# Performance work log

Measured on AMD Instinct MI355X. Metric: run time of the kernel, lower is better.

The kernel has to match this reference:

```python
import jax, jax.numpy as jnp
import numpy as np

SQRT_D = 32  # ceil(sqrt(d_out)) with d_out = 1024
D_OUT = 1024


def setup_inputs() -> dict:
    key = jax.random.key(0)
    k1, k2, k3 = jax.random.split(key, 3)
    x = jax.random.normal(k1, (8, 4096, 1024), dtype=jnp.float32)
    scale = 1.0 / np.sqrt(SQRT_D)
    L = jax.random.normal(k2, (SQRT_D, SQRT_D, SQRT_D), dtype=jnp.float32) * scale
    R = jax.random.normal(k3, (SQRT_D, SQRT_D, SQRT_D), dtype=jnp.float32) * scale
    return {"x": x, "L": L, "R": R}


def reference(x, L, R):
    # MonarchOutProjection with proj_type == 'Monarch' (d_in*n_heads == d_out,
    # hd == sqrt_d**2 so no padding). Monarch: permute -> blockdiag(L) ->
    # permute -> blockdiag(R) -> permute, then slice to d_out.
    b, n, hd = x.shape
    s = SQRT_D
    # rearrange '... (m n) -> ... (n m)': view (m, n) then transpose.
    h = x.reshape(b, n, s, s)          # (..., m, n_inner)
    h = jnp.swapaxes(h, -1, -2)        # (..., block, inner)
    # blockdiag_matmul with L: einsum 'bnm,...bm->...bn'
    h = jnp.einsum('bnm,...bm->...bn', L, h)
    # rearrange '... (m n) -> ... (n m)' on the flattened result == transpose
    h = jnp.swapaxes(h, -1, -2)
    # blockdiag_matmul with R
    h = jnp.einsum('bnm,...bm->...bn', R, h)
    # final rearrange '... (m n) -> ... (n m)'
    h = jnp.swapaxes(h, -1, -2)
    out = h.reshape(b, n, hd)
    return out[..., :D_OUT]
```

## Files before the change

### kernel.cpp

```cpp
#include <hip/hip_runtime.h>
#include <hip/hip_bf16.h>


typedef __attribute__((ext_vector_type(8))) short short8;
typedef __attribute__((ext_vector_type(4))) float floatx4;

__device__ __forceinline__ unsigned int f2bf(float f) {
    unsigned int u = __float_as_uint(f);
    return (u + 0x7fffu + ((u >> 16) & 1u)) >> 16;
}
__device__ __forceinline__ unsigned int pack2bf(float a, float b) {
    __hip_bfloat162 h = __float22bfloat162_rn(float2{a, b});
    return *(unsigned int*)&h;
}
__device__ __forceinline__ float bf2f(unsigned int u16) {
    return __uint_as_float(u16 << 16);
}

__global__ void prep_weights(const float* __restrict__ L, const float* __restrict__ R,
                             unsigned short* __restrict__ Lb, unsigned short* __restrict__ Rb) {
    const int t = blockIdx.x * 256 + threadIdx.x;
    const float* src        = (t < 4096) ? L : R;
    unsigned short* dst     = (t < 4096) ? Lb : Rb;
    const int i    = t & 4095;
    const int lane = i & 63;
    const int pq   = i >> 6;
    const int p    = pq >> 1;
    const int qt   = pq & 1;
    const int q    = qt * 16 + (lane & 15);
    const int m0   = (lane >> 4) * 8;
    const float* s = src + (p * 32 + q) * 32 + m0;
    uint4 o;
    o.x = pack2bf(s[0], s[1]);
    o.y = pack2bf(s[2], s[3]);
    o.z = pack2bf(s[4], s[5]);
    o.w = pack2bf(s[6], s[7]);
    *(uint4*)(dst + (size_t)i * 8) = o;
}

__global__ __launch_bounds__(256, 4)
void monarch_kernel(const float* __restrict__ x,
                    const unsigned short* __restrict__ Lb,
                    const unsigned short* __restrict__ Rb,
                    float* __restrict__ out) {
    __shared__ __align__(16) unsigned short buf[16][1024];

    const int tid  = threadIdx.x;
    const int w    = tid >> 6;
    const int lane = tid & 63;
    const int tl   = lane & 15;
    const int quad = lane >> 4;
    const long tok0 = (long)blockIdx.x * 16;

    {
        const int c = tid * 4;
        #pragma unroll
        for (int t = 0; t < 16; ++t) {
            const float4 v = *(const float4*)(x + (tok0 + t) * 1024 + c);
            *(unsigned int*)&buf[t][(c    ) ^ (2 * t)] = pack2bf(v.x, v.y);
            *(unsigned int*)&buf[t][(c + 2) ^ (2 * t)] = pack2bf(v.z, v.w);
        }
    }
    __syncthreads();

    {
        const int xsw = 2 * tl;
        #pragma unroll
        for (int pp = 0; pp < 8; ++pp) {
            const int p  = w * 8 + pp;
            const int pX = p ^ xsw;
            short8 b1;
            #pragma unroll
            for (int j = 0; j < 8; ++j)
                b1[j] = (short)buf[tl][quad * 256 + j * 32 + pX];
            #pragma unroll
            for (int qt = 0; qt < 2; ++qt) {
                const short8 a1 = *(const short8*)(Lb + (size_t)((p * 2 + qt) * 64 + lane) * 8);
                floatx4 acc = {0.f, 0.f, 0.f, 0.f};
                acc = __builtin_amdgcn_mfma_f32_16x16x32_bf16(a1, b1, acc, 0, 0, 0);
                #pragma unroll
                for (int r = 0; r < 4; ++r) {
                    const int qo = qt * 16 + quad * 4 + r;
                    buf[tl][qo * 32 + pX] = (unsigned short)f2bf(acc[r]);
                }
            }
        }
    }
    __syncthreads();

    floatx4 acc2[8][2];
    {
        const int xsw = 2 * tl;
        #pragma unroll
        for (int qq = 0; qq < 8; ++qq) {
            const int q = w * 8 + qq;
            short8 b2;
            #pragma unroll
            for (int j = 0; j < 8; ++j)
                b2[j] = (short)buf[tl][q * 32 + ((quad * 8 + j) ^ xsw)];
            #pragma unroll
            for (int rt = 0; rt < 2; ++rt) {
                const short8 a2 = *(const short8*)(Rb + (size_t)((q * 2 + rt) * 64 + lane) * 8);
                floatx4 z = {0.f, 0.f, 0.f, 0.f};
                acc2[qq][rt] = __builtin_amdgcn_mfma_f32_16x16x32_bf16(a2, b2, z, 0, 0, 0);
            }
        }
    }
    __syncthreads();

    {
        const int xsw = 2 * tl;
        #pragma unroll
        for (int qq = 0; qq < 8; ++qq) {
            const int q  = w * 8 + qq;
            const int qX = q ^ xsw;
            #pragma unroll
            for (int rt = 0; rt < 2; ++rt) {
                #pragma unroll
                for (int r4 = 0; r4 < 4; ++r4) {
                    const int ro = rt * 16 + quad * 4 + r4;
                    buf[tl][ro * 32 + qX] = (unsigned short)f2bf(acc2[qq][rt][r4]);
                }
            }
        }
    }
    __syncthreads();

    {
        const int c = tid * 4;
        #pragma unroll
        for (int t = 0; t < 16; ++t) {
            const unsigned int u0 = *(const unsigned int*)&buf[t][(c    ) ^ (2 * t)];
            const unsigned int u1 = *(const unsigned int*)&buf[t][(c + 2) ^ (2 * t)];
            float4 o;
            o.x = bf2f(u0 & 0xffffu); o.y = bf2f(u0 >> 16);
            o.z = bf2f(u1 & 0xffffu); o.w = bf2f(u1 >> 16);
            *(float4*)(out + (tok0 + t) * 1024 + c) = o;
        }
    }
}

extern "C" void kernel_launch(void* const* d_in, const int* in_sizes, int n_in,
                              void* d_out, int out_size, void* d_ws, size_t ws_size,
                              hipStream_t stream) {
    const float* x = (const float*)d_in[0];
    const float* L = (const float*)d_in[1];
    const float* R = (const float*)d_in[2];
    float* out = (float*)d_out;

    unsigned short* Lb = (unsigned short*)d_ws;
    unsigned short* Rb = Lb + 32768;

    prep_weights<<<32, 256, 0, stream>>>(L, R, Lb, Rb);

    const int n_tokens = 8 * 4096;
    const int grid = n_tokens / 16;
    monarch_kernel<<<grid, 256, 0, stream>>>(x, Lb, Rb, out);
}
```

Measured before the change: 242.1 us.

## Process two token tiles per block and prefetch the next tile's input during compute

Each block now handles 32 tokens in two iterations. The block loads the first tile's x into registers up front and issues the second tile's global loads during the first tile's second-stage matmul, which overlaps memory latency with compute. Stage-two results are packed to bf16 in registers, and the bf16 pack routine is swapped to a manual rounding version. The cost is more register pressure from 16 float4 values held across the loop, plus a halved grid, which may reduce occupancy and latency hiding under the 4-block launch bound.

```diff
diff --git a/kernel.cpp b/kernel.cpp
--- a/kernel.cpp
+++ b/kernel.cpp
@@ -10,8 +10,7 @@
     return (u + 0x7fffu + ((u >> 16) & 1u)) >> 16;
 }
 __device__ __forceinline__ unsigned int pack2bf(float a, float b) {
-    __hip_bfloat162 h = __float22bfloat162_rn(float2{a, b});
-    return *(unsigned int*)&h;
+    return f2bf(a) | (f2bf(b) << 16);
 }
 __device__ __forceinline__ float bf2f(unsigned int u16) {
     return __uint_as_float(u16 << 16);
@@ -50,84 +49,102 @@
     const int lane = tid & 63;
     const int tl   = lane & 15;
     const int quad = lane >> 4;
-    const long tok0 = (long)blockIdx.x * 16;
+    const int c    = tid * 4;
+    const long tokB = (long)blockIdx.x * 32;
 
-    {
-        const int c = tid * 4;
+    float4 v[16];
+    #pragma unroll
+    for (int t = 0; t < 16; ++t)
+        v[t] = *(const float4*)(x + (tokB + t) * 1024 + c);
+
+    #pragma unroll 1
+    for (int it = 0; it < 2; ++it) {
+        const long tok0 = tokB + it * 16;
+
         #pragma unroll
         for (int t = 0; t < 16; ++t) {
-            const float4 v = *(const float4*)(x + (tok0 + t) * 1024 + c);
-            *(unsigned int*)&buf[t][(c    ) ^ (2 * t)] = pack2bf(v.x, v.y);
-            *(unsigned int*)&buf[t][(c + 2) ^ (2 * t)] = pack2bf(v.z, v.w);
+            *(unsigned int*)&buf[t][(c    ) ^ (2 * t)] = pack2bf(v[t].x, v[t].y);
+            *(unsigned int*)&buf[t][(c + 2) ^ (2 * t)] = pack2bf(v[t].z, v[t].w);
         }
-    }
-    __syncthreads();
+        __syncthreads();
 
-    {
-        const int xsw = 2 * tl;
-        #pragma unroll
-        for (int pp = 0; pp < 8; ++pp) {
-            const int p  = w * 8 + pp;
-            const int pX = p ^ xsw;
-            short8 b1;
+        {
+            const int xsw = 2 * tl;
             #pragma unroll
-            for (int j = 0; j < 8; ++j)
-                b1[j] = (short)buf[tl][quad * 256 + j * 32 + pX];
-            #pragma unroll
-            for (int qt = 0; qt < 2; ++qt) {
-                const short8 a1 = *(const short8*)(Lb + (size_t)((p * 2 + qt) * 64 + lane) * 8);
-                floatx4 acc = {0.f, 0.f, 0.f, 0.f};
-                acc = __builtin_amdgcn_mfma_f32_16x16x32_bf16(a1, b1, acc, 0, 0, 0);
+            for (int pp = 0; pp < 8; ++pp) {
+                const int p  = w * 8 + pp;
+                const int pX = p ^ xsw;
+                short8 b1;
                 #pragma unroll
-                for (int r = 0; r < 4; ++r) {
-                    const int qo = qt * 16 + quad * 4 + r;
-                    buf[tl][qo * 32 + pX] = (unsigned short)f2bf(acc[r]);
+                for (int j = 0; j < 8; ++j)
+                    b1[j] = (short)buf[tl][quad * 256 + j * 32 + pX];
+                #pragma unroll
+                for (int qt = 0; qt < 2; ++qt) {
+                    const short8 a1 = *(const short8*)(Lb + (size_t)((p * 2 + qt) * 64 + lane) * 8);
+                    floatx4 acc = {0.f, 0.f, 0.f, 0.f};
+                    acc = __builtin_amdgcn_mfma_f32_16x16x32_bf16(a1, b1, acc, 0, 0, 0);
+                    #pragma unroll
+                    for (int r = 0; r < 4; ++r) {
+                        const int qo = qt * 16 + quad * 4 + r;
+                        buf[tl][qo * 32 + pX] = (unsigned short)f2bf(acc[r]);
+                    }
                 }
             }
         }
-    }
-    __syncthreads();
+        __syncthreads();
 
-    floatx4 acc2[8][2];
-    {
-        const int xsw = 2 * tl;
-        #pragma unroll
-        for (int qq = 0; qq < 8; ++qq) {
-            const int q = w * 8 + qq;
-            short8 b2;
+        if (it == 0) {
             #pragma unroll
-            for (int j = 0; j < 8; ++j)
-                b2[j] = (short)buf[tl][q * 32 + ((quad * 8 + j) ^ xsw)];
+            for (int t = 0; t < 8; ++t)
+                v[t] = *(const float4*)(x + (tokB + 16 + t) * 1024 + c);
+        }
+
+        unsigned int y2p[8][2][2];
+        {
+            const int xsw = 2 * tl;
             #pragma unroll
-            for (int rt = 0; rt < 2; ++rt) {
-                const short8 a2 = *(const short8*)(Rb + (size_t)((q * 2 + rt) * 64 + lane) * 8);
-                floatx4 z = {0.f, 0.f, 0.f, 0.f};
-                acc2[qq][rt] = __builtin_amdgcn_mfma_f32_16x16x32_bf16(a2, b2, z, 0, 0, 0);
-            }
-        }
-    }
-    __syncthreads();
-
-    {
-        const int xsw = 2 * tl;
-        #pragma unroll
-        for (int qq = 0; qq < 8; ++qq) {
-            const int q  = w * 8 + qq;
-            const int qX = q ^ xsw;
-            #pragma unroll
-            for (int rt = 0; rt < 2; ++rt) {
+            for (int qq = 0; qq < 8; ++qq) {
+                const int q = w * 8 + qq;
+                short8 b2;
                 #pragma unroll
-                for (int r4 = 0; r4 < 4; ++r4) {
-                    const int ro = rt * 16 + quad * 4 + r4;
-                    buf[tl][ro * 32 + qX] = (unsigned short)f2bf(acc2[qq][rt][r4]);
+                for (int j = 0; j < 8; ++j)
+                    b2[j] = (short)buf[tl][q * 32 + ((quad * 8 + j) ^ xsw)];
+                #pragma unroll
+                for (int rt = 0; rt < 2; ++rt) {
+                    const short8 a2 = *(const short8*)(Rb + (size_t)((q * 2 + rt) * 64 + lane) * 8);
+                    floatx4 z = {0.f, 0.f, 0.f, 0.f};
+                    floatx4 acc = __builtin_amdgcn_mfma_f32_16x16x32_bf16(a2, b2, z, 0, 0, 0);
+                    y2p[qq][rt][0] = pack2bf(acc[0], acc[1]);
+                    y2p[qq][rt][1] = pack2bf(acc[2], acc[3]);
                 }
             }
         }
-    }
-    __syncthreads();
 
-    {
-        const int c = tid * 4;
+        if (it == 0) {
+            #pragma unroll
+            for (int t = 8; t < 16; ++t)
+                v[t] = *(const float4*)(x + (tokB + 16 + t) * 1024 + c);
+        }
+        __syncthreads();
+
+        {
+            const int xsw = 2 * tl;
+            #pragma unroll
+            for (int qq = 0; qq < 8; ++qq) {
+                const int q  = w * 8 + qq;
+                const int qX = q ^ xsw;
+                #pragma unroll
+                for (int rt = 0; rt < 2; ++rt) {
+                    const int ro = rt * 16 + quad * 4;
+                    buf[tl][(ro    ) * 32 + qX] = (unsigned short)(y2p[qq][rt][0] & 0xffffu);
+                    buf[tl][(ro + 1) * 32 + qX] = (unsigned short)(y2p[qq][rt][0] >> 16);
+                    buf[tl][(ro + 2) * 32 + qX] = (unsigned short)(y2p[qq][rt][1] & 0xffffu);
+                    buf[tl][(ro + 3) * 32 + qX] = (unsigned short)(y2p[qq][rt][1] >> 16);
+                }
+            }
+        }
+        __syncthreads();
+
         #pragma unroll
         for (int t = 0; t < 16; ++t) {
             const unsigned int u0 = *(const unsigned int*)&buf[t][(c    ) ^ (2 * t)];
@@ -137,6 +154,7 @@
             o.z = bf2f(u1 & 0xffffu); o.w = bf2f(u1 >> 16);
             *(float4*)(out + (tok0 + t) * 1024 + c) = o;
         }
+        __syncthreads();
     }
 }
 
@@ -153,7 +171,6 @@
 
     prep_weights<<<32, 256, 0, stream>>>(L, R, Lb, Rb);
 
-    const int n_tokens = 8 * 4096;
-    const int grid = n_tokens / 16;
+    const int grid = 1024;
     monarch_kernel<<<grid, 256, 0, stream>>>(x, Lb, Rb, out);
 }
```

Result: slower. 418.9 us (+73.0%).
